# Optimization experiments

Measured on AMD Instinct MI355X. Metric: run time of the kernel, lower is better.

## Reference

```python
import jax, jax.numpy as jnp
import numpy as np

L_LAYERS = 2
EPS = 1e-6  # flax LayerNorm default epsilon


def _binop_reset(qi, qj):
    # S5 resettable associative scan element: (A, Bu, reset_flag)
    Ai, bi, ci = qi
    Aj, bj, cj = qj
    A = (Aj * Ai) * (1 - cj) + Aj * cj
    b = (Aj * bi + bj) * (1 - cj) + bj * cj
    c = ci * (1 - cj) + cj
    return A, b, c


def _layernorm(x, scale, bias):
    mu = jnp.mean(x, axis=-1, keepdims=True)
    var = jnp.var(x, axis=-1, keepdims=True)
    return (x - mu) * jax.lax.rsqrt(var + EPS) * scale + bias


def _s5_layer(x, resets, h0, lam_re, lam_im, B2, C2, Dv, log_step, nsc, nbi, gw, gb):
    # x: (B,T,H) float32; resets: (B,T) float32; h0: (B,1,P) complex64
    Bsz, T, H = x.shape
    P = lam_re.shape[0]
    skip = x
    xn = _layernorm(x, nsc, nbi)
    # ZOH discretization
    Lam = lam_re + 1j * lam_im                       # (P,)
    step = jnp.exp(log_step[:, 0])                   # (P,)
    Lam_bar = jnp.exp(Lam * step)                    # (P,)
    B_t = B2[..., 0] + 1j * B2[..., 1]               # (P,H)
    B_bar = ((Lam_bar - 1.0) / Lam)[:, None] * B_t   # (P,H)
    C_t = C2[..., 0] + 1j * C2[..., 1]               # (H,P)
    Bu = jnp.einsum('ph,bth->btp', B_bar, xn.astype(B_bar.dtype))  # (B,T,P) complex
    # prepend carry / identity elements, run reset-aware parallel scan over time
    ones = jnp.ones((Bsz, 1, P), dtype=Lam_bar.dtype)
    A_el = jnp.concatenate([ones, jnp.broadcast_to(Lam_bar, (Bsz, T, P))], axis=1)
    b_el = jnp.concatenate([h0, Bu], axis=1)
    c_el = jnp.concatenate([jnp.zeros((Bsz, 1, 1), x.dtype), resets[..., None]], axis=1)
    _, xs, _ = jax.lax.associative_scan(_binop_reset, (A_el, b_el, c_el), axis=1)
    xs = xs[:, 1:]                                   # (B,T,P) states
    h_new = xs[:, -1:, :]                            # (B,1,P) new carry
    ys = 2.0 * jnp.einsum('hp,btp->bth', C_t, xs).real  # conj_sym output
    y = ys + Dv * xn                                 # skip-through D
    # half_glu1 activation
    y = jax.nn.gelu(y)
    y = y * jax.nn.sigmoid(y @ gw + gb)
    return h_new, skip + y


def setup_inputs() -> dict:
    key = jax.random.key(0)
    B, T, OBS, H, P, L = 128, 1024, 512, 64, 128, L_LAYERS
    ks = jax.random.split(key, 10)
    obs = jax.random.normal(ks[0], (B, T, OBS), jnp.float32)
    dones = (jax.random.uniform(ks[1], (B, T)) < 0.02).astype(jnp.int32)
    hidden = jnp.zeros((L, B, 1, P, 2), jnp.float32)
    dense_w = jax.random.normal(ks[2], (OBS, H), jnp.float32) * np.float32(1.0 / np.sqrt(OBS))
    dense_b = jnp.zeros((H,), jnp.float32)
    Lambda_re = -(0.5 + jax.random.uniform(ks[3], (L, P), jnp.float32))  # stable (negative) real parts
    Lambda_im = np.float32(np.pi) * jax.random.normal(ks[4], (L, P), jnp.float32)
    Bp = jax.random.normal(ks[5], (L, P, H, 2), jnp.float32) * np.float32(1.0 / np.sqrt(H))
    Cp = jax.random.normal(ks[6], (L, H, P, 2), jnp.float32) * np.float32(1.0 / np.sqrt(P))
    D = jax.random.normal(ks[7], (L, H), jnp.float32)
    log_step = jax.random.uniform(ks[8], (L, P, 1), jnp.float32,
                                  minval=np.float32(np.log(0.001)), maxval=np.float32(np.log(0.1)))
    norm_scale = jnp.ones((L, H), jnp.float32)
    norm_bias = jnp.zeros((L, H), jnp.float32)
    glu_w = jax.random.normal(ks[9], (L, H, H), jnp.float32) * np.float32(1.0 / np.sqrt(H))
    glu_b = jnp.zeros((L, H), jnp.float32)
    return {"obs": obs, "dones": dones, "hidden": hidden, "dense_w": dense_w, "dense_b": dense_b,
            "Lambda_re": Lambda_re, "Lambda_im": Lambda_im, "Bp": Bp, "Cp": Cp, "D": D,
            "log_step": log_step, "norm_scale": norm_scale, "norm_bias": norm_bias,
            "glu_w": glu_w, "glu_b": glu_b}


def reference(obs, dones, hidden, dense_w, dense_b, Lambda_re, Lambda_im, Bp, Cp, D,
              log_step, norm_scale, norm_bias, glu_w, glu_b):
    x = obs @ dense_w + dense_b                      # dense_0 embedding (B,T,H)
    resets = dones.astype(x.dtype)
    h = hidden[..., 0] + 1j * hidden[..., 1]         # (L,B,1,P) complex carries
    new_h = []
    for l in range(L_LAYERS):
        hl, x = _s5_layer(x, resets, h[l], Lambda_re[l], Lambda_im[l], Bp[l], Cp[l], D[l],
                          log_step[l], norm_scale[l], norm_bias[l], glu_w[l], glu_b[l])
        new_h.append(hl)
    h_out = jnp.stack(new_h, axis=0)                 # (L,B,1,P) complex
    h_out = jnp.stack([h_out.real, h_out.imag], axis=-1)
    return h_out, x
```

## Files before the change

kernel.cpp:

```cpp
#include <hip/hip_runtime.h>

#define NB 128
#define NT 1024
#define NOBS 512
#define NH 64
#define NP 128
#define NM (NB*NT)
#define NN2 256
#define NCH 16
#define CHL 64

typedef short bf16x8 __attribute__((ext_vector_type(8)));
typedef float f32x4 __attribute__((ext_vector_type(4)));

#define BU_OFF    ((size_t)0)
#define AGGA_OFF  ((size_t)83886080)
#define AGGB_OFF  ((size_t)85983232)
#define AGGC_OFF  ((size_t)88080384)
#define HIN_OFF   ((size_t)89128960)
#define CONST_OFF ((size_t)91226112)
#define CONST_STRIDE ((size_t)131072)
#define WTB_OFF   ((size_t)92274688)

__device__ __forceinline__ unsigned short f2b(float f) {
  unsigned int u = __float_as_uint(f);
  u = u + 0x7fffu + ((u >> 16) & 1u);
  return (unsigned short)(u >> 16);
}
__device__ __forceinline__ float b2f(unsigned short s) {
  return __uint_as_float(((unsigned int)s) << 16);
}

__global__ __launch_bounds__(256) void k_setup(const float* Lre, const float* Lim,
    const float* Bp, const float* Cp, const float* lstep, const float* gw,
    const float* dw, unsigned char* wsb) {
  int l = blockIdx.y;
  int idx = blockIdx.x * 256 + threadIdx.x;
  unsigned char* cb = wsb + CONST_OFF + (size_t)l * CONST_STRIDE;
  float2* lambar = (float2*)cb;
  unsigned short* Bglob = (unsigned short*)(cb + 1024);
  unsigned short* Cglob = (unsigned short*)(cb + 33792);
  unsigned short* gwT   = (unsigned short*)(cb + 66560);
  {
    int n = idx >> 6, h = idx & 63, p = n >> 1, c = n & 1;
    float step = expf(lstep[l * NP + p]);
    float re = Lre[l * NP + p], im = Lim[l * NP + p];
    float er = expf(re * step), ang = im * step;
    float lbr = er * cosf(ang), lbi = er * sinf(ang);
    if (h == 0 && c == 0) lambar[p] = make_float2(lbr, lbi);
    float den = re * re + im * im;
    float nr = lbr - 1.f, ni = lbi;
    float dr = (nr * re + ni * im) / den;
    float di = (ni * re - nr * im) / den;
    size_t bb = ((size_t)(l * NP + p) * NH + h) * 2;
    float b0 = Bp[bb + 0], b1 = Bp[bb + 1];
    float vr = dr * b0 - di * b1;
    float vi = dr * b1 + di * b0;
    Bglob[n * 64 + h] = f2b(c ? vi : vr);
  }
  {
    int h = idx >> 8, n = idx & 255, p = n >> 1;
    size_t base = ((size_t)(l * NH + h) * NP + p) * 2;
    float val = (n & 1) ? (-2.f * Cp[base + 1]) : (2.f * Cp[base + 0]);
    Cglob[h * 256 + n] = f2b(val);
  }
  if (idx < 4096) {
    int n = idx >> 6, k = idx & 63;
    gwT[n * 64 + k] = f2b(gw[(size_t)(l * NH + k) * NH + n]);
  }
  {
    int idx2 = l * 16384 + idx;
    int h = idx2 >> 9, k = idx2 & 511;
    ((unsigned short*)(wsb + WTB_OFF))[h * 512 + k] = f2b(dw[(size_t)k * NH + h]);
  }
}

__global__ __launch_bounds__(256) void k_dense(const float* __restrict__ obs,
    const unsigned short* __restrict__ wTb, const float* __restrict__ bias,
    float* __restrict__ xout) {
  __shared__ __align__(16) unsigned short As[128][72];
  __shared__ __align__(16) unsigned short Bs[64][72];
  int tid = threadIdx.x, lane = tid & 63, wv = tid >> 6;
  int row0 = blockIdx.x * 128;
  f32x4 acc[2][4] = {};
  float bcol[4];
#pragma unroll
  for (int ct = 0; ct < 4; ++ct) bcol[ct] = bias[ct * 16 + (lane & 15)];
  float4 ra[8];
  uint4 rb[2];
#pragma unroll
  for (int i = 0; i < 8; ++i) {
    int id = tid + i * 256;
    ra[i] = *(const float4*)(obs + (size_t)(row0 + (id >> 4)) * NOBS + (id & 15) * 4);
  }
#pragma unroll
  for (int i = 0; i < 2; ++i) {
    int id = tid + i * 256;
    rb[i] = *(const uint4*)(wTb + (id >> 3) * 512 + (id & 7) * 8);
  }
  for (int kt = 0; kt < 8; ++kt) {
#pragma unroll
    for (int i = 0; i < 8; ++i) {
      int id = tid + i * 256;
      ushort4 o; o.x = f2b(ra[i].x); o.y = f2b(ra[i].y); o.z = f2b(ra[i].z); o.w = f2b(ra[i].w);
      *(ushort4*)&As[id >> 4][(id & 15) * 4] = o;
    }
#pragma unroll
    for (int i = 0; i < 2; ++i) {
      int id = tid + i * 256;
      *(uint4*)&Bs[id >> 3][(id & 7) * 8] = rb[i];
    }
    __syncthreads();
    if (kt < 7) {
      int k0 = (kt + 1) * 64;
#pragma unroll
      for (int i = 0; i < 8; ++i) {
        int id = tid + i * 256;
        ra[i] = *(const float4*)(obs + (size_t)(row0 + (id >> 4)) * NOBS + k0 + (id & 15) * 4);
      }
#pragma unroll
      for (int i = 0; i < 2; ++i) {
        int id = tid + i * 256;
        rb[i] = *(const uint4*)(wTb + (id >> 3) * 512 + k0 + (id & 7) * 8);
      }
    }
#pragma unroll
    for (int kc = 0; kc < 2; ++kc) {
      bf16x8 a0 = *(const bf16x8*)&As[wv * 32 + (lane & 15)][kc * 32 + (lane >> 4) * 8];
      bf16x8 a1 = *(const bf16x8*)&As[wv * 32 + 16 + (lane & 15)][kc * 32 + (lane >> 4) * 8];
#pragma unroll
      for (int ct = 0; ct < 4; ++ct) {
        bf16x8 bb = *(const bf16x8*)&Bs[ct * 16 + (lane & 15)][kc * 32 + (lane >> 4) * 8];
        acc[0][ct] = __builtin_amdgcn_mfma_f32_16x16x32_bf16(a0, bb, acc[0][ct], 0, 0, 0);
        acc[1][ct] = __builtin_amdgcn_mfma_f32_16x16x32_bf16(a1, bb, acc[1][ct], 0, 0, 0);
      }
    }
    __syncthreads();
  }
  float* Os = (float*)&As[0][0];
#pragma unroll
  for (int pass = 0; pass < 2; ++pass) {
    if ((wv >> 1) == pass) {
#pragma unroll
      for (int rt = 0; rt < 2; ++rt)
#pragma unroll
        for (int ct = 0; ct < 4; ++ct)
#pragma unroll
          for (int e = 0; e < 4; ++e) {
            int rl = (wv & 1) * 32 + rt * 16 + (lane >> 4) * 4 + e;
            int col = ct * 16 + (lane & 15);
            Os[rl * 68 + col] = acc[rt][ct][e] + bcol[ct];
          }
    }
    __syncthreads();
    {
      int r = tid >> 2, seg = tid & 3;
#pragma unroll
      for (int i = 0; i < 4; ++i)
        *(float4*)(xout + (size_t)(row0 + pass * 64 + r) * NH + seg * 16 + i * 4) =
            *(const float4*)&Os[r * 68 + seg * 16 + i * 4];
    }
    __syncthreads();
  }
}

__global__ __launch_bounds__(256) void k_lnbu_scan1(const float* __restrict__ x,
    const float* __restrict__ nsc, const float* __restrict__ nbi,
    const unsigned char* __restrict__ cb, const int* __restrict__ dones,
    unsigned short* __restrict__ bu,
    float2* __restrict__ aggA, float2* __restrict__ aggB, float* __restrict__ aggC) {
  __shared__ __align__(16) unsigned short BuS[64][264];
  __shared__ __align__(16) unsigned short Bs[256][72];
  __shared__ int dS[64];
  __shared__ float pA[256][2], pB[256][2], pC[256];
  unsigned short (*As)[72] = (unsigned short (*)[72])&BuS[0][0];
  int tid = threadIdx.x, lane = tid & 63, wv = tid >> 6;
  int row0 = blockIdx.x * 64;
  int b = blockIdx.x >> 4, ch = blockIdx.x & 15;
  const unsigned short* Bglob = (const unsigned short*)(cb + 1024);
  {
    const unsigned short* src = Bglob + tid * 64;
#pragma unroll
    for (int i = 0; i < 8; ++i)
      *(uint4*)&Bs[tid][i * 8] = *(const uint4*)(src + i * 8);
  }
  if (tid < 64) dS[tid] = dones[b * NT + ch * CHL + tid];
  {
    int r = tid >> 2, q = tid & 3;
    const float* xr = x + (size_t)(row0 + r) * NH + q * 16;
    float4 vv[4];
#pragma unroll
    for (int i = 0; i < 4; ++i) vv[i] = *(const float4*)(xr + i * 4);
    const float* vp = (const float*)vv;
    float s = 0.f, s2 = 0.f;
#pragma unroll
    for (int j = 0; j < 16; ++j) { s += vp[j]; s2 += vp[j] * vp[j]; }
    s += __shfl_xor(s, 1); s2 += __shfl_xor(s2, 1);
    s += __shfl_xor(s, 2); s2 += __shfl_xor(s2, 2);
    float mu = s * 0.015625f;
    float var = s2 * 0.015625f - mu * mu;
    float rs = rsqrtf(var + 1e-6f);
#pragma unroll
    for (int j = 0; j < 16; ++j) {
      float xv = (vp[j] - mu) * rs * nsc[q * 16 + j] + nbi[q * 16 + j];
      As[r][q * 16 + j] = f2b(xv);
    }
  }
  __syncthreads();
  f32x4 acc[16] = {};
#pragma unroll
  for (int kc = 0; kc < 2; ++kc) {
    bf16x8 a = *(const bf16x8*)&As[wv * 16 + (lane & 15)][kc * 32 + (lane >> 4) * 8];
#pragma unroll
    for (int ct = 0; ct < 16; ++ct) {
      bf16x8 bb = *(const bf16x8*)&Bs[ct * 16 + (lane & 15)][kc * 32 + (lane >> 4) * 8];
      acc[ct] = __builtin_amdgcn_mfma_f32_16x16x32_bf16(a, bb, acc[ct], 0, 0, 0);
    }
  }
  __syncthreads();
#pragma unroll
  for (int ct = 0; ct < 16; ++ct)
#pragma unroll
    for (int e = 0; e < 4; ++e)
      BuS[wv * 16 + (lane >> 4) * 4 + e][ct * 16 + (lane & 15)] = f2b(acc[ct][e]);
  __syncthreads();
  {
    int r = tid >> 2, seg = tid & 3;
#pragma unroll
    for (int i = 0; i < 8; ++i)
      *(uint4*)(bu + (size_t)(row0 + r) * NN2 + seg * 64 + i * 8) =
          *(const uint4*)&BuS[r][seg * 64 + i * 8];
  }
  {
    int p = tid & 127, half = tid >> 7;
    float2 lam = ((const float2*)cb)[p];
    float Ar = 1.f, Ai = 0.f, br = 0.f, bi = 0.f, c = 0.f;
    int t0 = half * 32;
#pragma unroll 4
    for (int i = 0; i < 32; ++i) {
      int t = t0 + i;
      unsigned int u = *(const unsigned int*)&BuS[t][2 * p];
      float bur = b2f((unsigned short)(u & 0xffffu));
      float bui = b2f((unsigned short)(u >> 16));
      if (dS[t]) { Ar = lam.x; Ai = lam.y; br = bur; bi = bui; c = 1.f; }
      else {
        float nAr = lam.x * Ar - lam.y * Ai; Ai = lam.x * Ai + lam.y * Ar; Ar = nAr;
        float nbr = lam.x * br - lam.y * bi + bur; bi = lam.x * bi + lam.y * br + bui; br = nbr;
      }
    }
    pA[tid][0] = Ar; pA[tid][1] = Ai; pB[tid][0] = br; pB[tid][1] = bi; pC[tid] = c;
  }
  __syncthreads();
  if (tid < 128) {
    float A0r = pA[tid][0], A0i = pA[tid][1], b0r = pB[tid][0], b0i = pB[tid][1], c0 = pC[tid];
    float A1r = pA[tid + 128][0], A1i = pA[tid + 128][1];
    float b1r = pB[tid + 128][0], b1i = pB[tid + 128][1], c1 = pC[tid + 128];
    float Ar, Ai, br, bi, c;
    if (c1 != 0.f) { Ar = A1r; Ai = A1i; br = b1r; bi = b1i; c = 1.f; }
    else {
      Ar = A1r * A0r - A1i * A0i; Ai = A1r * A0i + A1i * A0r;
      br = A1r * b0r - A1i * b0i + b1r; bi = A1r * b0i + A1i * b0r + b1i;
      c = c0;
    }
    int o = (b * NCH + ch) * NP + tid;
    aggA[o] = make_float2(Ar, Ai);
    aggB[o] = make_float2(br, bi);
    aggC[o] = c;
  }
}

__global__ __launch_bounds__(256) void k_scanchunks(const float* __restrict__ hidden,
    const float2* __restrict__ aggA, const float2* __restrict__ aggB,
    const float* __restrict__ aggC, float2* __restrict__ hin,
    float* __restrict__ hout, int l) {
  int gid = blockIdx.x * 256 + threadIdx.x;
  int b = gid >> 7, p = gid & 127;
  size_t hoff = ((size_t)(l * NB + b) * NP + p) * 2;
  float hr = hidden[hoff], hi = hidden[hoff + 1];
  for (int ch = 0; ch < NCH; ++ch) {
    int o = (b * NCH + ch) * NP + p;
    hin[o] = make_float2(hr, hi);
    float2 A = aggA[o]; float2 bb = aggB[o]; float c = aggC[o];
    if (c != 0.f) { hr = bb.x; hi = bb.y; }
    else {
      float nr = A.x * hr - A.y * hi + bb.x;
      hi = A.x * hi + A.y * hr + bb.y; hr = nr;
    }
  }
  hout[hoff] = hr; hout[hoff + 1] = hi;
}

__global__ __launch_bounds__(256) void k_ysglu_scan2(const unsigned short* __restrict__ bu,
    const int* __restrict__ dones, const unsigned char* __restrict__ cb,
    const float2* __restrict__ hin,
    const float* __restrict__ nsc, const float* __restrict__ nbi,
    const float* __restrict__ Dv, const float* __restrict__ gb,
    float* __restrict__ x) {
  __shared__ __align__(16) unsigned short BuS[64][264];
  __shared__ __align__(16) unsigned short Cs[64][264];
  __shared__ __align__(16) unsigned short Gs[64][72];
  __shared__ float muS[64], rsS[64];
  __shared__ int dS[64];
  unsigned short (*Ys)[72] = (unsigned short (*)[72])&BuS[0][0];
  float* Os = (float*)&Cs[0][0];
  int tid = threadIdx.x, lane = tid & 63, wv = tid >> 6;
  int row0 = blockIdx.x * 64;
  int b = blockIdx.x >> 4, ch = blockIdx.x & 15;
  const unsigned short* Cglob = (const unsigned short*)(cb + 33792);
  const unsigned short* gwT = (const unsigned short*)(cb + 66560);
  {
    int r = tid >> 2, seg = tid & 3;
#pragma unroll
    for (int i = 0; i < 8; ++i)
      *(uint4*)&BuS[r][seg * 64 + i * 8] =
          *(const uint4*)(bu + (size_t)(row0 + r) * NN2 + seg * 64 + i * 8);
  }
  {
    int h = tid >> 2, n0 = (tid & 3) * 64;
#pragma unroll
    for (int i = 0; i < 8; ++i)
      *(uint4*)&Cs[h][n0 + i * 8] = *(const uint4*)(Cglob + h * 256 + n0 + i * 8);
  }
  {
    int n = tid >> 2, k0 = (tid & 3) * 16;
#pragma unroll
    for (int i = 0; i < 2; ++i)
      *(uint4*)&Gs[n][k0 + i * 8] = *(const uint4*)(gwT + n * 64 + k0 + i * 8);
  }
  if (tid < 64) dS[tid] = dones[b * NT + ch * CHL + tid];
  float2 hseed;
  if (tid < 128) hseed = hin[(b * NCH + ch) * NP + tid];
  float xreg[4][4];
#pragma unroll
  for (int ct = 0; ct < 4; ++ct)
#pragma unroll
    for (int e = 0; e < 4; ++e) {
      int rl = wv * 16 + (lane >> 4) * 4 + e;
      xreg[ct][e] = x[(size_t)(row0 + rl) * NH + ct * 16 + (lane & 15)];
    }
  {
    int r = tid >> 2, q = tid & 3;
    const float* xr = x + (size_t)(row0 + r) * NH + q * 16;
    float4 vv[4];
#pragma unroll
    for (int i = 0; i < 4; ++i) vv[i] = *(const float4*)(xr + i * 4);
    const float* vp = (const float*)vv;
    float s = 0.f, s2 = 0.f;
#pragma unroll
    for (int j = 0; j < 16; ++j) { s += vp[j]; s2 += vp[j] * vp[j]; }
    s += __shfl_xor(s, 1); s2 += __shfl_xor(s2, 1);
    s += __shfl_xor(s, 2); s2 += __shfl_xor(s2, 2);
    float mu = s * 0.015625f;
    float var = s2 * 0.015625f - mu * mu;
    if (q == 0) { muS[r] = mu; rsS[r] = rsqrtf(var + 1e-6f); }
  }
  __syncthreads();
  if (tid < 128) {
    int p = tid;
    float2 lam = ((const float2*)cb)[p];
    float hr = hseed.x, hi = hseed.y;
#pragma unroll 4
    for (int t = 0; t < CHL; ++t) {
      unsigned int u = *(const unsigned int*)&BuS[t][2 * p];
      float bur = b2f((unsigned short)(u & 0xffffu));
      float bui = b2f((unsigned short)(u >> 16));
      if (dS[t]) { hr = bur; hi = bui; }
      else {
        float nr = lam.x * hr - lam.y * hi + bur;
        hi = lam.x * hi + lam.y * hr + bui; hr = nr;
      }
      *(unsigned int*)&BuS[t][2 * p] = (unsigned int)f2b(hr) | ((unsigned int)f2b(hi) << 16);
    }
  }
  __syncthreads();
  f32x4 acc[4] = {};
#pragma unroll
  for (int kc = 0; kc < 8; ++kc) {
    bf16x8 a = *(const bf16x8*)&BuS[wv * 16 + (lane & 15)][kc * 32 + (lane >> 4) * 8];
#pragma unroll
    for (int ct = 0; ct < 4; ++ct) {
      bf16x8 bb = *(const bf16x8*)&Cs[ct * 16 + (lane & 15)][kc * 32 + (lane >> 4) * 8];
      acc[ct] = __builtin_amdgcn_mfma_f32_16x16x32_bf16(a, bb, acc[ct], 0, 0, 0);
    }
  }
  __syncthreads();
  float yreg[4][4];
#pragma unroll
  for (int ct = 0; ct < 4; ++ct)
#pragma unroll
    for (int e = 0; e < 4; ++e) {
      int rl = wv * 16 + (lane >> 4) * 4 + e;
      int col = ct * 16 + (lane & 15);
      float xnv = (xreg[ct][e] - muS[rl]) * rsS[rl] * nsc[col] + nbi[col];
      float yv = acc[ct][e] + Dv[col] * xnv;
      float t3 = 0.7978845608f * (yv + 0.044715f * yv * yv * yv);
      yv = 0.5f * yv * (1.f + tanhf(t3));
      yreg[ct][e] = yv;
      Ys[rl][col] = f2b(yv);
    }
  __syncthreads();
  f32x4 gacc[4] = {};
#pragma unroll
  for (int kc = 0; kc < 2; ++kc) {
    bf16x8 a = *(const bf16x8*)&Ys[wv * 16 + (lane & 15)][kc * 32 + (lane >> 4) * 8];
#pragma unroll
    for (int ct = 0; ct < 4; ++ct) {
      bf16x8 bb = *(const bf16x8*)&Gs[ct * 16 + (lane & 15)][kc * 32 + (lane >> 4) * 8];
      gacc[ct] = __builtin_amdgcn_mfma_f32_16x16x32_bf16(a, bb, gacc[ct], 0, 0, 0);
    }
  }
#pragma unroll
  for (int ct = 0; ct < 4; ++ct)
#pragma unroll
    for (int e = 0; e < 4; ++e) {
      int rl = wv * 16 + (lane >> 4) * 4 + e;
      int col = ct * 16 + (lane & 15);
      float g = gacc[ct][e] + gb[col];
      float s = 1.f / (1.f + expf(-g));
      Os[rl * 66 + col] = xreg[ct][e] + yreg[ct][e] * s;
    }
  __syncthreads();
  {
    int r = tid >> 2, seg = tid & 3;
#pragma unroll
    for (int i = 0; i < 4; ++i)
      *(float4*)(x + (size_t)(row0 + r) * NH + seg * 16 + i * 4) =
          *(const float4*)&Os[r * 66 + seg * 16 + i * 4];
  }
}

extern "C" void kernel_launch(void* const* d_in, const int* in_sizes, int n_in,
                              void* d_out, int out_size, void* d_ws, size_t ws_size,
                              hipStream_t stream) {
  const float* obs    = (const float*)d_in[0];
  const int*   dones  = (const int*)d_in[1];
  const float* hidden = (const float*)d_in[2];
  const float* dw     = (const float*)d_in[3];
  const float* db     = (const float*)d_in[4];
  const float* Lre    = (const float*)d_in[5];
  const float* Lim    = (const float*)d_in[6];
  const float* Bp     = (const float*)d_in[7];
  const float* Cp     = (const float*)d_in[8];
  const float* Dv     = (const float*)d_in[9];
  const float* lstep  = (const float*)d_in[10];
  const float* nsc    = (const float*)d_in[11];
  const float* nbi    = (const float*)d_in[12];
  const float* gw     = (const float*)d_in[13];
  const float* gb     = (const float*)d_in[14];

  float* hout = (float*)d_out;
  float* x = hout + (size_t)2 * NB * NP * 2;

  unsigned char* wsb = (unsigned char*)d_ws;
  unsigned short* bu = (unsigned short*)(wsb + BU_OFF);
  float2* aggA = (float2*)(wsb + AGGA_OFF);
  float2* aggB = (float2*)(wsb + AGGB_OFF);
  float*  aggC = (float*)(wsb + AGGC_OFF);
  float2* hin  = (float2*)(wsb + HIN_OFF);
  unsigned short* wTb = (unsigned short*)(wsb + WTB_OFF);

  k_setup<<<dim3(64, 2), 256, 0, stream>>>(Lre, Lim, Bp, Cp, lstep, gw, dw, wsb);
  k_dense<<<NM / 128, 256, 0, stream>>>(obs, wTb, db, x);
  for (int l = 0; l < 2; ++l) {
    const unsigned char* cb = wsb + CONST_OFF + (size_t)l * CONST_STRIDE;
    k_lnbu_scan1<<<NM / 64, 256, 0, stream>>>(x, nsc + l * NH, nbi + l * NH, cb, dones,
                                              bu, aggA, aggB, aggC);
    k_scanchunks<<<NB * NP / 256, 256, 0, stream>>>(hidden, aggA, aggB, aggC, hin, hout, l);
    k_ysglu_scan2<<<NM / 64, 256, 0, stream>>>(bu, dones, cb, hin,
                                               nsc + l * NH, nbi + l * NH,
                                               Dv + l * NH, gb + l * NH, x);
  }
}
```

Baseline: 330.8 us.

## Read MFMA weight fragments from global memory, shrink LDS, use fast exp math

The two per-layer kernels no longer stage the B, C and GLU weight matrices in shared memory. MFMA B-operand fragments are now read directly from global memory, relying on L1/L2 caching since every block uses the same weights. This cuts LDS use per block and adds launch_bounds(256,4), aiming to fit more blocks per CU. GELU's tanhf is replaced with an __expf-based formula and sigmoid uses __expf, trading a little precision and more global/L2 load traffic on the inner MFMA loop for cheaper math and higher occupancy.

```diff
diff --git a/kernel.cpp b/kernel.cpp
--- a/kernel.cpp
+++ b/kernel.cpp
@@ -164,13 +164,12 @@
   }
 }
 
-__global__ __launch_bounds__(256) void k_lnbu_scan1(const float* __restrict__ x,
+__global__ __launch_bounds__(256, 4) void k_lnbu_scan1(const float* __restrict__ x,
     const float* __restrict__ nsc, const float* __restrict__ nbi,
     const unsigned char* __restrict__ cb, const int* __restrict__ dones,
     unsigned short* __restrict__ bu,
     float2* __restrict__ aggA, float2* __restrict__ aggB, float* __restrict__ aggC) {
   __shared__ __align__(16) unsigned short BuS[64][264];
-  __shared__ __align__(16) unsigned short Bs[256][72];
   __shared__ int dS[64];
   __shared__ float pA[256][2], pB[256][2], pC[256];
   unsigned short (*As)[72] = (unsigned short (*)[72])&BuS[0][0];
@@ -178,12 +177,6 @@
   int row0 = blockIdx.x * 64;
   int b = blockIdx.x >> 4, ch = blockIdx.x & 15;
   const unsigned short* Bglob = (const unsigned short*)(cb + 1024);
-  {
-    const unsigned short* src = Bglob + tid * 64;
-#pragma unroll
-    for (int i = 0; i < 8; ++i)
-      *(uint4*)&Bs[tid][i * 8] = *(const uint4*)(src + i * 8);
-  }
   if (tid < 64) dS[tid] = dones[b * NT + ch * CHL + tid];
   {
     int r = tid >> 2, q = tid & 3;
@@ -213,7 +206,7 @@
     bf16x8 a = *(const bf16x8*)&As[wv * 16 + (lane & 15)][kc * 32 + (lane >> 4) * 8];
 #pragma unroll
     for (int ct = 0; ct < 16; ++ct) {
-      bf16x8 bb = *(const bf16x8*)&Bs[ct * 16 + (lane & 15)][kc * 32 + (lane >> 4) * 8];
+      bf16x8 bb = *(const bf16x8*)(Bglob + (ct * 16 + (lane & 15)) * 64 + kc * 32 + (lane >> 4) * 8);
       acc[ct] = __builtin_amdgcn_mfma_f32_16x16x32_bf16(a, bb, acc[ct], 0, 0, 0);
     }
   }
@@ -290,19 +283,17 @@
   hout[hoff] = hr; hout[hoff + 1] = hi;
 }
 
-__global__ __launch_bounds__(256) void k_ysglu_scan2(const unsigned short* __restrict__ bu,
+__global__ __launch_bounds__(256, 4) void k_ysglu_scan2(const unsigned short* __restrict__ bu,
     const int* __restrict__ dones, const unsigned char* __restrict__ cb,
     const float2* __restrict__ hin,
     const float* __restrict__ nsc, const float* __restrict__ nbi,
     const float* __restrict__ Dv, const float* __restrict__ gb,
     float* __restrict__ x) {
   __shared__ __align__(16) unsigned short BuS[64][264];
-  __shared__ __align__(16) unsigned short Cs[64][264];
-  __shared__ __align__(16) unsigned short Gs[64][72];
   __shared__ float muS[64], rsS[64];
   __shared__ int dS[64];
   unsigned short (*Ys)[72] = (unsigned short (*)[72])&BuS[0][0];
-  float* Os = (float*)&Cs[0][0];
+  float* Os = (float*)((char*)&BuS[0][0] + 16384);
   int tid = threadIdx.x, lane = tid & 63, wv = tid >> 6;
   int row0 = blockIdx.x * 64;
   int b = blockIdx.x >> 4, ch = blockIdx.x & 15;
@@ -314,18 +305,6 @@
     for (int i = 0; i < 8; ++i)
       *(uint4*)&BuS[r][seg * 64 + i * 8] =
           *(const uint4*)(bu + (size_t)(row0 + r) * NN2 + seg * 64 + i * 8);
-  }
-  {
-    int h = tid >> 2, n0 = (tid & 3) * 64;
-#pragma unroll
-    for (int i = 0; i < 8; ++i)
-      *(uint4*)&Cs[h][n0 + i * 8] = *(const uint4*)(Cglob + h * 256 + n0 + i * 8);
-  }
-  {
-    int n = tid >> 2, k0 = (tid & 3) * 16;
-#pragma unroll
-    for (int i = 0; i < 2; ++i)
-      *(uint4*)&Gs[n][k0 + i * 8] = *(const uint4*)(gwT + n * 64 + k0 + i * 8);
   }
   if (tid < 64) dS[tid] = dones[b * NT + ch * CHL + tid];
   float2 hseed;
@@ -379,7 +358,7 @@
     bf16x8 a = *(const bf16x8*)&BuS[wv * 16 + (lane & 15)][kc * 32 + (lane >> 4) * 8];
 #pragma unroll
     for (int ct = 0; ct < 4; ++ct) {
-      bf16x8 bb = *(const bf16x8*)&Cs[ct * 16 + (lane & 15)][kc * 32 + (lane >> 4) * 8];
+      bf16x8 bb = *(const bf16x8*)(Cglob + (ct * 16 + (lane & 15)) * 256 + kc * 32 + (lane >> 4) * 8);
       acc[ct] = __builtin_amdgcn_mfma_f32_16x16x32_bf16(a, bb, acc[ct], 0, 0, 0);
     }
   }
@@ -394,7 +373,9 @@
       float xnv = (xreg[ct][e] - muS[rl]) * rsS[rl] * nsc[col] + nbi[col];
       float yv = acc[ct][e] + Dv[col] * xnv;
       float t3 = 0.7978845608f * (yv + 0.044715f * yv * yv * yv);
-      yv = 0.5f * yv * (1.f + tanhf(t3));
+      float u = __expf(2.f * t3);
+      float th = 1.f - 2.f / (u + 1.f);
+      yv = 0.5f * yv * (1.f + th);
       yreg[ct][e] = yv;
       Ys[rl][col] = f2b(yv);
     }
@@ -405,7 +386,7 @@
     bf16x8 a = *(const bf16x8*)&Ys[wv * 16 + (lane & 15)][kc * 32 + (lane >> 4) * 8];
 #pragma unroll
     for (int ct = 0; ct < 4; ++ct) {
-      bf16x8 bb = *(const bf16x8*)&Gs[ct * 16 + (lane & 15)][kc * 32 + (lane >> 4) * 8];
+      bf16x8 bb = *(const bf16x8*)(gwT + (ct * 16 + (lane & 15)) * 64 + kc * 32 + (lane >> 4) * 8);
       gacc[ct] = __builtin_amdgcn_mfma_f32_16x16x32_bf16(a, bb, gacc[ct], 0, 0, 0);
     }
   }
@@ -416,7 +397,7 @@
       int rl = wv * 16 + (lane >> 4) * 4 + e;
       int col = ct * 16 + (lane & 15);
       float g = gacc[ct][e] + gb[col];
-      float s = 1.f / (1.f + expf(-g));
+      float s = 1.f / (1.f + __expf(-g));
       Os[rl * 66 + col] = xreg[ct][e] + yreg[ct][e] * s;
     }
   __syncthreads();
```

Result: slower. 346.3 us (+4.7%).
